# Kernel tuning notes

Hardware: AMD Instinct MI355X
Metric: run time of the kernel (lower is better)

The kernel has to match this reference:

```python
import jax, jax.numpy as jnp
import numpy as np

N, E, D, H, Z, HEADS = 20000, 160000, 3000, 512, 50, 3
EPS = 1e-5


def _bn(x, gamma, beta):
    # BatchNorm1d, training-mode stats (biased variance), eps=1e-5
    m = x.mean(axis=0)
    v = x.var(axis=0)
    return (x - m) * jax.lax.rsqrt(v + EPS) * gamma + beta


def _gat(x, src, dst, n, W, att_src, att_dst, bias, heads, c):
    # PyG GATConv, concat=False (mean over heads), negative_slope=0.2
    h = (x @ W).reshape(n, heads, c)                      # [N,H,C]
    a_s = (h * att_src).sum(-1)                           # [N,H]
    a_d = (h * att_dst).sum(-1)                           # [N,H]
    e = jax.nn.leaky_relu(a_s[src] + a_d[dst], 0.2)       # [Etot,H]
    e = e - jax.ops.segment_max(e, dst, num_segments=n)[dst]
    ex = jnp.exp(e)
    den = jax.ops.segment_sum(ex, dst, num_segments=n)[dst]
    alpha = ex / den                                      # segment softmax over incoming edges
    msg = h[src] * alpha[:, :, None]                      # [Etot,H,C]
    out = jax.ops.segment_sum(msg, dst, num_segments=n)   # [N,H,C]
    return out.mean(axis=1) + bias


def setup_inputs() -> dict:
    key = jax.random.key(0)
    ks = jax.random.split(key, 16)
    s = 0.05
    inp = {
        "x": jax.random.normal(ks[0], (N, D), dtype=jnp.float32),
        "edge_index": jax.random.randint(ks[1], (2, E), 0, N, dtype=jnp.int64),
        "W1": jax.random.normal(ks[2], (D, HEADS * H), dtype=jnp.float32) * s,
        "att_src1": jax.random.normal(ks[3], (HEADS, H), dtype=jnp.float32) * s,
        "att_dst1": jax.random.normal(ks[4], (HEADS, H), dtype=jnp.float32) * s,
        "b1": jnp.zeros((H,), jnp.float32),
        "bn1_g": jnp.ones((H,), jnp.float32),
        "bn1_b": jnp.zeros((H,), jnp.float32),
        "W2": jax.random.normal(ks[5], (H, HEADS * Z), dtype=jnp.float32) * s,
        "att_src2": jax.random.normal(ks[6], (HEADS, Z), dtype=jnp.float32) * s,
        "att_dst2": jax.random.normal(ks[7], (HEADS, Z), dtype=jnp.float32) * s,
        "b2": jnp.zeros((Z,), jnp.float32),
        "bn2_g": jnp.ones((Z,), jnp.float32),
        "bn2_b": jnp.zeros((Z,), jnp.float32),
        "lin1_w": jax.random.normal(ks[8], (H, Z), dtype=jnp.float32) * s,
        "lin1_b": jnp.zeros((H,), jnp.float32),
        "dbn_g": jnp.ones((H,), jnp.float32),
        "dbn_b": jnp.zeros((H,), jnp.float32),
        "lin2_w": jax.random.normal(ks[9], (D, H), dtype=jnp.float32) * s,
        "lin2_b": jnp.zeros((D,), jnp.float32),
    }
    return inp


def reference(x, edge_index, W1, att_src1, att_dst1, b1, bn1_g, bn1_b,
              W2, att_src2, att_dst2, b2, bn2_g, bn2_b,
              lin1_w, lin1_b, dbn_g, dbn_b, lin2_w, lin2_b):
    n = x.shape[0]
    loop = jnp.arange(n, dtype=edge_index.dtype)
    src = jnp.concatenate([edge_index[0], loop])  # add self-loops (PyG default)
    dst = jnp.concatenate([edge_index[1], loop])
    h = jax.nn.relu(_bn(_gat(x, src, dst, n, W1, att_src1, att_dst1, b1, HEADS, H), bn1_g, bn1_b))
    z = jax.nn.relu(_bn(_gat(h, src, dst, n, W2, att_src2, att_dst2, b2, HEADS, Z), bn2_g, bn2_b))
    d = jax.nn.relu(_bn(z @ lin1_w.T + lin1_b, dbn_g, dbn_b))
    out = jax.nn.relu(d @ lin2_w.T + lin2_b)
    return out
```

## Files before the change

kernel.cpp:

```cpp
#include <hip/hip_runtime.h>
#include <stdint.h>

typedef unsigned short u16;
typedef __attribute__((ext_vector_type(8))) short s16x8;
typedef __attribute__((ext_vector_type(4))) short s16x4;
typedef __attribute__((ext_vector_type(4))) float f32x4;

#define DEVFN static __device__ __forceinline__

static constexpr int NN = 20000;
static constexpr int EE = 160000;
static constexpr int ET = 180000;
static constexpr int DD = 3000;
static constexpr int HH = 512;
static constexpr int ZZ = 50;
static constexpr int C1 = 1536;
static constexpr int C2 = 150;
static constexpr int KP1 = 3008;

DEVFN u16 f2b(float f) {
  uint32_t u = __builtin_bit_cast(uint32_t, f);
  u += 0x7FFFu + ((u >> 16) & 1u);
  return (u16)(u >> 16);
}
DEVFN float b2f(u16 b) {
  uint32_t u = ((uint32_t)b) << 16;
  return __builtin_bit_cast(float, u);
}
DEVFN int edge_at(const void* ei, int mode32, long idx) {
  return mode32 ? ((const int*)ei)[idx] : (int)((const long long*)ei)[idx];
}

typedef __attribute__((address_space(1))) const unsigned int gas_uint;
typedef __attribute__((address_space(3))) unsigned int las_uint;
DEVFN void async16(const u16* g, u16* l) {
  __builtin_amdgcn_global_load_lds((gas_uint*)(uintptr_t)g,
                                   (las_uint*)(unsigned)(uintptr_t)l, 16, 0, 0);
}

__global__ void k_detect(const int* __restrict__ ei, int* __restrict__ mode) {
  __shared__ int nz;
  if (threadIdx.x == 0) nz = 0;
  __syncthreads();
  int loc = 0;
  for (int i = threadIdx.x; i < 1024; i += blockDim.x)
    if (ei[2 * i + 1] != 0) loc = 1;
  if (loc) atomicOr(&nz, 1);
  __syncthreads();
  if (threadIdx.x == 0) *mode = nz;
}

__global__ void k_deg(const void* ei, const int* __restrict__ mode, int* __restrict__ deg) {
  int m = *mode;
  long i = (long)blockIdx.x * blockDim.x + threadIdx.x;
  long st = (long)gridDim.x * blockDim.x;
  for (; i < ET; i += st) {
    int d = (i < EE) ? edge_at(ei, m, EE + i) : (int)(i - EE);
    if ((unsigned)d < (unsigned)NN) atomicAdd(&deg[d], 1);
  }
}

__global__ void k_scan_blk(const int* __restrict__ deg, int* __restrict__ rowptr,
                           int* __restrict__ bsum) {
  __shared__ int buf[256];
  int b = blockIdx.x, tid = threadIdx.x;
  int i = b * 256 + tid;
  buf[tid] = (i < NN) ? deg[i] : 0;
  __syncthreads();
  for (int off = 1; off < 256; off <<= 1) {
    int t = (tid >= off) ? buf[tid - off] : 0;
    __syncthreads();
    buf[tid] += t;
    __syncthreads();
  }
  if (i < NN) rowptr[i + 1] = buf[tid];
  if (tid == 255) bsum[b] = buf[255];
}
__global__ void k_scan_top(int* __restrict__ bsum, int nb) {
  __shared__ int buf[128];
  int tid = threadIdx.x;
  buf[tid] = (tid < nb) ? bsum[tid] : 0;
  __syncthreads();
  for (int off = 1; off < 128; off <<= 1) {
    int t = (tid >= off) ? buf[tid - off] : 0;
    __syncthreads();
    buf[tid] += t;
    __syncthreads();
  }
  if (tid < nb) bsum[tid] = buf[tid];
}
__global__ void k_scan_add(int* __restrict__ rowptr, const int* __restrict__ bsum) {
  int b = blockIdx.x, tid = threadIdx.x;
  int i = b * 256 + tid;
  if (i == 0) rowptr[0] = 0;
  if (b > 0 && i < NN) rowptr[i + 1] += bsum[b - 1];
}

__global__ void k_fill(const void* ei, const int* __restrict__ mode,
                       const int* __restrict__ rowptr, int* __restrict__ cursor,
                       int* __restrict__ srcp) {
  int m = *mode;
  long i = (long)blockIdx.x * blockDim.x + threadIdx.x;
  long st = (long)gridDim.x * blockDim.x;
  for (; i < ET; i += st) {
    int s, d;
    if (i < EE) { s = edge_at(ei, m, i); d = edge_at(ei, m, EE + i); }
    else { s = d = (int)(i - EE); }
    if ((unsigned)d < (unsigned)NN && (unsigned)s < (unsigned)NN) {
      int pos = atomicAdd(&cursor[d], 1);
      srcp[rowptr[d] + pos] = s;
    }
  }
}

__global__ void k_cvt_pad4(const float* __restrict__ in, u16* __restrict__ out,
                           int R, int Cin, int ldo) {
  int r = blockIdx.y;
  int c = (blockIdx.x * blockDim.x + threadIdx.x) * 4;
  if (c >= ldo) return;
  s16x4 o;
  const float* src = in + (size_t)r * Cin + c;
  if (r < R && c + 4 <= Cin && ((((size_t)r * Cin + c) & 3) == 0)) {
    f32x4 v = *(const f32x4*)src;
#pragma unroll
    for (int j = 0; j < 4; j++) o[j] = (short)f2b(v[j]);
  } else {
#pragma unroll
    for (int j = 0; j < 4; j++)
      o[j] = (short)((r < R && c + j < Cin) ? f2b(src[j]) : (u16)0);
  }
  *(s16x4*)(out + (size_t)r * ldo + c) = o;
}

__global__ void k_transpose_tile(const float* __restrict__ in, u16* __restrict__ out,
                                 int R, int Cc, int ldo) {
  __shared__ float t[32][33];
  int tx = threadIdx.x & 31, ty = threadIdx.x >> 5;
  int c0 = blockIdx.x * 32, r0 = blockIdx.y * 32;
#pragma unroll
  for (int j = 0; j < 4; j++) {
    int r = r0 + ty + j * 8, c = c0 + tx;
    t[ty + j * 8][tx] = (r < R && c < Cc) ? in[(size_t)r * Cc + c] : 0.f;
  }
  __syncthreads();
#pragma unroll
  for (int j = 0; j < 4; j++) {
    int c = c0 + ty + j * 8, r = r0 + tx;
    if (c < Cc && r < ldo) out[(size_t)c * ldo + r] = f2b(t[tx][ty + j * 8]);
  }
}

__global__ void k_transpose_cvt2(const float* __restrict__ in, u16* __restrict__ out,
                                 int R, int C, int Cp, int ldo) {
  long total = (long)Cp * ldo;
  long i = (long)blockIdx.x * blockDim.x + threadIdx.x;
  long st = (long)gridDim.x * blockDim.x;
  for (; i < total; i += st) {
    int c = (int)(i / ldo), r = (int)(i % ldo);
    out[i] = (c < C && r < R) ? f2b(in[(size_t)r * C + c]) : (u16)0;
  }
}

template<bool OUT_BF16, bool RELU>
__global__ __launch_bounds__(256) void k_gemm3(
    const u16* __restrict__ Ag, const u16* __restrict__ Bg, void* __restrict__ Cg,
    const float* __restrict__ bias, int M, int Nn, int Kp, int ld, int ldc) {
  __shared__ __align__(16) u16 As[2][128][64];
  __shared__ __align__(16) u16 Bs[2][128][64];
  int tid = threadIdx.x;
  int lane = tid & 63, wid = tid >> 6;
  int wm = wid >> 1, wn = wid & 1;
  int lr = lane & 15, lg = lane >> 4;

  int nwg = gridDim.x * gridDim.y;
  int wg = blockIdx.y * gridDim.x + blockIdx.x;
  int q = nwg >> 3, r = nwg & 7;
  int xcd = wg & 7, loc = wg >> 3;
  int swz = (xcd < r ? xcd * (q + 1) : r * (q + 1) + (xcd - r) * q) + loc;
  int m0 = (swz / gridDim.x) * 128, n0 = (swz % gridDim.x) * 128;

  int srow = lane >> 3;
  int skk = ((lane & 7) ^ srow) * 8;
  const u16* agp[4];
  const u16* bgp[4];
#pragma unroll
  for (int i = 0; i < 4; i++) {
    int ra = wid * 32 + i * 8 + srow;
    int ga = m0 + ra; if (ga > M - 1) ga = M - 1;
    agp[i] = Ag + (size_t)ga * ld + skk;
    bgp[i] = Bg + (size_t)(n0 + ra) * ld + skk;
  }

#define STAGE(bufi, kofs) do {                                   \
    u16* la_ = &As[bufi][0][0] + wid * 2048;                     \
    u16* lb_ = &Bs[bufi][0][0] + wid * 2048;                     \
    _Pragma("unroll")                                            \
    for (int i_ = 0; i_ < 4; i_++) {                             \
      async16(agp[i_] + (kofs), la_ + i_ * 512);                 \
      async16(bgp[i_] + (kofs), lb_ + i_ * 512);                 \
    }                                                            \
  } while (0)

  f32x4 acc[4][4];
#pragma unroll
  for (int mi = 0; mi < 4; mi++)
#pragma unroll
    for (int ni = 0; ni < 4; ni++) {
      acc[mi][ni][0] = 0.f; acc[mi][ni][1] = 0.f; acc[mi][ni][2] = 0.f; acc[mi][ni][3] = 0.f;
    }

  int rx = lr & 7;
  int NT = Kp >> 6;
  STAGE(0, 0);
  for (int t = 0; t < NT; t++) {
    int cur = t & 1;
    if (t + 1 < NT) {
      STAGE(cur ^ 1, (t + 1) * 64);
      asm volatile("s_waitcnt vmcnt(8)" ::: "memory");
    } else {
      asm volatile("s_waitcnt vmcnt(0)" ::: "memory");
    }
    __builtin_amdgcn_s_barrier();
    asm volatile("" ::: "memory");
#pragma unroll
    for (int ks = 0; ks < 2; ks++) {
      int ch = ((ks * 4 + lg) ^ rx) * 8;
      s16x8 a[4], b[4];
#pragma unroll
      for (int mi = 0; mi < 4; mi++)
        a[mi] = *(const s16x8*)&As[cur][wm * 64 + mi * 16 + lr][ch];
#pragma unroll
      for (int ni = 0; ni < 4; ni++)
        b[ni] = *(const s16x8*)&Bs[cur][wn * 64 + ni * 16 + lr][ch];
#pragma unroll
      for (int mi = 0; mi < 4; mi++)
#pragma unroll
        for (int ni = 0; ni < 4; ni++)
          acc[mi][ni] = __builtin_amdgcn_mfma_f32_16x16x32_bf16(a[mi], b[ni], acc[mi][ni], 0, 0, 0);
    }
    asm volatile("" ::: "memory");
    __builtin_amdgcn_s_barrier();
  }
#undef STAGE

#pragma unroll
  for (int mi = 0; mi < 4; mi++)
#pragma unroll
    for (int ni = 0; ni < 4; ni++) {
      int col = n0 + wn * 64 + ni * 16 + lr;
      if (col >= Nn) continue;
      float bv = bias ? bias[col] : 0.f;
#pragma unroll
      for (int j = 0; j < 4; j++) {
        int row = m0 + wm * 64 + mi * 16 + lg * 4 + j;
        if (row >= M) continue;
        float v = acc[mi][ni][j] + bv;
        if (RELU) v = v > 0.f ? v : 0.f;
        if (OUT_BF16) ((u16*)Cg)[(size_t)row * ldc + col] = f2b(v);
        else          ((float*)Cg)[(size_t)row * ldc + col] = v;
      }
    }
}

__global__ void k_attdot1b(const u16* __restrict__ h1b, const float* __restrict__ asrc,
                           const float* __restrict__ adst, float* __restrict__ as_,
                           float* __restrict__ ad_, float* __restrict__ z0,
                           float* __restrict__ z1) {
  int n = blockIdx.x;
  if (n == 0) {
    for (int i = threadIdx.x; i < HH; i += 192) { z0[i] = 0.f; z1[i] = 0.f; }
  }
  int hd = threadIdx.x >> 6, lane = threadIdx.x & 63;
  s16x8 h = *(const s16x8*)(h1b + (size_t)n * C1 + hd * 512 + lane * 8);
  const float* ap = asrc + hd * 512 + lane * 8;
  const float* dp = adst + hd * 512 + lane * 8;
  f32x4 a0 = *(const f32x4*)ap, a1 = *(const f32x4*)(ap + 4);
  f32x4 d0 = *(const f32x4*)dp, d1 = *(const f32x4*)(dp + 4);
  float ps = 0.f, pd = 0.f;
#pragma unroll
  for (int j = 0; j < 4; j++) {
    float hv = b2f((u16)h[j]);
    ps += hv * a0[j]; pd += hv * d0[j];
    float hw = b2f((u16)h[j + 4]);
    ps += hw * a1[j]; pd += hw * d1[j];
  }
  for (int off = 32; off; off >>= 1) { ps += __shfl_xor(ps, off); pd += __shfl_xor(pd, off); }
  if (lane == 0) { as_[3 * n + hd] = ps; ad_[3 * n + hd] = pd; }
}

__global__ void k_attdot2(const float* __restrict__ s2, const float* __restrict__ asrc,
                          const float* __restrict__ adst, float* __restrict__ as_,
                          float* __restrict__ ad_, float* __restrict__ z0,
                          float* __restrict__ z1, float* __restrict__ z2,
                          float* __restrict__ z3) {
  int n = blockIdx.x, tid = threadIdx.x;
  if (n == 0) {
    for (int i = tid; i < HH; i += 64) { z2[i] = 0.f; z3[i] = 0.f; }
    if (tid < 50) { z0[tid] = 0.f; z1[tid] = 0.f; }
  }
  for (int hd = 0; hd < 3; hd++) {
    float ps = 0.f, pd = 0.f;
    if (tid < 50) {
      float v = s2[(size_t)n * C2 + hd * 50 + tid];
      ps = v * asrc[hd * 50 + tid];
      pd = v * adst[hd * 50 + tid];
    }
    for (int off = 32; off; off >>= 1) { ps += __shfl_xor(ps, off); pd += __shfl_xor(pd, off); }
    if (tid == 0) { as_[3 * n + hd] = ps; ad_[3 * n + hd] = pd; }
  }
}

__global__ __launch_bounds__(192) void k_gat1(
    const u16* __restrict__ h1b, const float* __restrict__ as1,
    const float* __restrict__ ad1, const int* __restrict__ rowptr,
    const int* __restrict__ srcp, const float* __restrict__ bias,
    float* __restrict__ out) {
  int n = blockIdx.x, tid = threadIdx.x;
  __shared__ float sm[3], sden[3];
  __shared__ int s_src[128];
  __shared__ float s_alpha[128][3];
  __shared__ float part[3][512];
  int r0 = rowptr[n], deg = rowptr[n + 1] - r0;
  float adl[3] = {ad1[3 * n], ad1[3 * n + 1], ad1[3 * n + 2]};

  if (tid < 64) {
    float mx[3] = {-1e30f, -1e30f, -1e30f};
    for (int e = tid; e < deg; e += 64) {
      int s = srcp[r0 + e];
#pragma unroll
      for (int hd = 0; hd < 3; hd++) {
        float v = as1[3 * s + hd] + adl[hd];
        v = v > 0.f ? v : 0.2f * v;
        mx[hd] = fmaxf(mx[hd], v);
      }
    }
#pragma unroll
    for (int hd = 0; hd < 3; hd++)
      for (int off = 32; off; off >>= 1) mx[hd] = fmaxf(mx[hd], __shfl_xor(mx[hd], off));
    float sd[3] = {0.f, 0.f, 0.f};
    for (int e = tid; e < deg; e += 64) {
      int s = srcp[r0 + e];
#pragma unroll
      for (int hd = 0; hd < 3; hd++) {
        float v = as1[3 * s + hd] + adl[hd];
        v = v > 0.f ? v : 0.2f * v;
        sd[hd] += __expf(v - mx[hd]);
      }
    }
#pragma unroll
    for (int hd = 0; hd < 3; hd++)
      for (int off = 32; off; off >>= 1) sd[hd] += __shfl_xor(sd[hd], off);
    if (tid == 0) {
#pragma unroll
      for (int hd = 0; hd < 3; hd++) { sm[hd] = mx[hd]; sden[hd] = sd[hd]; }
    }
  }
  __syncthreads();

  int hd = tid >> 6, lane = tid & 63;
  float a[8];
#pragma unroll
  for (int j = 0; j < 8; j++) a[j] = 0.f;

  for (int base = 0; base < deg; base += 128) {
    int cnt = min(128, deg - base);
    if (tid < cnt) {
      int s = srcp[r0 + base + tid];
      s_src[tid] = s;
#pragma unroll
      for (int h2 = 0; h2 < 3; h2++) {
        float v = as1[3 * s + h2] + adl[h2];
        v = v > 0.f ? v : 0.2f * v;
        s_alpha[tid][h2] = __expf(v - sm[h2]) / sden[h2];
      }
    }
    __syncthreads();
    int e = 0;
    for (; e + 2 <= cnt; e += 2) {
      const u16* p0 = h1b + (size_t)s_src[e] * C1 + (hd << 9) + lane * 8;
      const u16* p1 = h1b + (size_t)s_src[e + 1] * C1 + (hd << 9) + lane * 8;
      s16x8 v0 = *(const s16x8*)p0;
      s16x8 v1 = *(const s16x8*)p1;
      float al0 = s_alpha[e][hd], al1 = s_alpha[e + 1][hd];
#pragma unroll
      for (int j = 0; j < 8; j++)
        a[j] += al0 * b2f((u16)v0[j]) + al1 * b2f((u16)v1[j]);
    }
    if (e < cnt) {
      const u16* p0 = h1b + (size_t)s_src[e] * C1 + (hd << 9) + lane * 8;
      s16x8 v0 = *(const s16x8*)p0;
      float al0 = s_alpha[e][hd];
#pragma unroll
      for (int j = 0; j < 8; j++) a[j] += al0 * b2f((u16)v0[j]);
    }
    __syncthreads();
  }

#pragma unroll
  for (int j = 0; j < 8; j++) part[hd][lane * 8 + j] = a[j];
  __syncthreads();
  if (tid < 128) {
    f32x4 p0 = *(const f32x4*)&part[0][tid * 4];
    f32x4 p1 = *(const f32x4*)&part[1][tid * 4];
    f32x4 p2 = *(const f32x4*)&part[2][tid * 4];
    f32x4 bv = *(const f32x4*)(bias + tid * 4);
    f32x4 o;
#pragma unroll
    for (int j = 0; j < 4; j++) o[j] = (p0[j] + p1[j] + p2[j]) * (1.f / 3.f) + bv[j];
    *(f32x4*)(out + (size_t)n * 512 + tid * 4) = o;
  }
}

__global__ void k_gat2(const float* __restrict__ s2, const float* __restrict__ as2,
                       const float* __restrict__ ad2, const int* __restrict__ rowptr,
                       const int* __restrict__ srcp, const float* __restrict__ bias,
                       float* __restrict__ z) {
  int n = blockIdx.x, tid = threadIdx.x;
  __shared__ int s_src[64];
  __shared__ float s_alpha[64][3];
  int r0 = rowptr[n], deg = rowptr[n + 1] - r0;
  float adl[3] = {ad2[3 * n], ad2[3 * n + 1], ad2[3 * n + 2]};

  float mx[3] = {-1e30f, -1e30f, -1e30f};
  for (int e = tid; e < deg; e += 64) {
    int s = srcp[r0 + e];
#pragma unroll
    for (int hd = 0; hd < 3; hd++) {
      float v = as2[3 * s + hd] + adl[hd];
      v = v > 0.f ? v : 0.2f * v;
      mx[hd] = fmaxf(mx[hd], v);
    }
  }
#pragma unroll
  for (int hd = 0; hd < 3; hd++)
    for (int off = 32; off; off >>= 1) mx[hd] = fmaxf(mx[hd], __shfl_xor(mx[hd], off));
  float sd[3] = {0.f, 0.f, 0.f};
  for (int e = tid; e < deg; e += 64) {
    int s = srcp[r0 + e];
#pragma unroll
    for (int hd = 0; hd < 3; hd++) {
      float v = as2[3 * s + hd] + adl[hd];
      v = v > 0.f ? v : 0.2f * v;
      sd[hd] += __expf(v - mx[hd]);
    }
  }
#pragma unroll
  for (int hd = 0; hd < 3; hd++)
    for (int off = 32; off; off >>= 1) sd[hd] += __shfl_xor(sd[hd], off);

  float acc = 0.f;
  for (int base = 0; base < deg; base += 64) {
    int cnt = min(64, deg - base);
    if (tid < cnt) {
      int s = srcp[r0 + base + tid];
      s_src[tid] = s;
#pragma unroll
      for (int hd = 0; hd < 3; hd++) {
        float v = as2[3 * s + hd] + adl[hd];
        v = v > 0.f ? v : 0.2f * v;
        s_alpha[tid][hd] = __expf(v - mx[hd]) / sd[hd];
      }
    }
    __syncthreads();
    if (tid < 50) {
      for (int e = 0; e < cnt; e++) {
        const float* row = s2 + (size_t)s_src[e] * C2;
#pragma unroll
        for (int hd = 0; hd < 3; hd++) acc += s_alpha[e][hd] * row[hd * 50 + tid];
      }
    }
    __syncthreads();
  }
  if (tid < 50) z[(size_t)n * ZZ + tid] = acc * (1.f / 3.f) + bias[tid];
}

__global__ void k_colstats3(const float* __restrict__ x, float* __restrict__ gsum,
                            float* __restrict__ gsq, long total, int C) {
  long i = (long)blockIdx.x * blockDim.x + threadIdx.x;
  long st = (long)gridDim.x * blockDim.x;
  int c = (int)(i % C);
  float s = 0.f, q = 0.f;
  for (; i < total; i += st) { float v = x[i]; s += v; q += v * v; }
  atomicAdd(&gsum[c], s);
  atomicAdd(&gsq[c], q);
}

__global__ void k_bnfinal(const float* __restrict__ gsum, const float* __restrict__ gsq,
                          const float* __restrict__ g, const float* __restrict__ b,
                          float* __restrict__ scale, float* __restrict__ shift,
                          int C, float invN) {
  int c = blockIdx.x * blockDim.x + threadIdx.x;
  if (c < C) {
    float m = gsum[c] * invN;
    float var = gsq[c] * invN - m * m;
    float rs = rsqrtf(var + 1e-5f);
    float sc = g[c] * rs;
    scale[c] = sc;
    shift[c] = b[c] - m * sc;
  }
}

__global__ void k_bnrelu4(const float* __restrict__ x, const float* __restrict__ sc,
                          const float* __restrict__ sh, u16* __restrict__ out, long total4) {
  long i = (long)blockIdx.x * blockDim.x + threadIdx.x;
  long st = (long)gridDim.x * blockDim.x;
  for (; i < total4; i += st) {
    long b = i * 4;
    int c = (int)(b & 511);
    f32x4 v = *(const f32x4*)(x + b);
    f32x4 s = *(const f32x4*)(sc + c);
    f32x4 t = *(const f32x4*)(sh + c);
    s16x4 o;
#pragma unroll
    for (int j = 0; j < 4; j++) {
      float r = v[j] * s[j] + t[j];
      r = r > 0.f ? r : 0.f;
      o[j] = (short)f2b(r);
    }
    *(s16x4*)(out + b) = o;
  }
}

__global__ void k_bnrelu_pad(const float* __restrict__ x, const float* __restrict__ sc,
                             const float* __restrict__ sh, u16* __restrict__ out) {
  int i = blockIdx.x * blockDim.x + threadIdx.x;
  if (i >= NN * 64) return;
  int c = i & 63, r = i >> 6;
  float v = 0.f;
  if (c < 50) {
    v = x[r * 50 + c] * sc[c] + sh[c];
    v = v > 0.f ? v : 0.f;
  }
  out[i] = f2b(v);
}

extern "C" void kernel_launch(void* const* d_in, const int* in_sizes, int n_in,
                              void* d_out, int out_size, void* d_ws, size_t ws_size,
                              hipStream_t stream) {
  (void)in_sizes; (void)n_in; (void)out_size;
  const float* x     = (const float*)d_in[0];
  const void*  ei    = d_in[1];
  const float* W1    = (const float*)d_in[2];
  const float* asrc1 = (const float*)d_in[3];
  const float* adst1 = (const float*)d_in[4];
  const float* b1    = (const float*)d_in[5];
  const float* bn1g  = (const float*)d_in[6];
  const float* bn1b  = (const float*)d_in[7];
  const float* W2    = (const float*)d_in[8];
  const float* asrc2 = (const float*)d_in[9];
  const float* adst2 = (const float*)d_in[10];
  const float* b2    = (const float*)d_in[11];
  const float* bn2g  = (const float*)d_in[12];
  const float* bn2b  = (const float*)d_in[13];
  const float* l1w   = (const float*)d_in[14];
  const float* l1b   = (const float*)d_in[15];
  const float* dbng  = (const float*)d_in[16];
  const float* dbnb  = (const float*)d_in[17];
  const float* l2w   = (const float*)d_in[18];
  const float* l2b   = (const float*)d_in[19];
  float* out = (float*)d_out;
  char* ws = (char*)d_ws;

  size_t off = 0;
  auto alloc = [&](size_t b) { size_t r = off; off += (b + 255) & ~(size_t)255; return r; };
  const size_t oXB  = alloc(120320000);
  const size_t oH1  = alloc(61440000);
  const size_t oW1T = alloc((size_t)C1 * KP1 * 2);
  const size_t oAS1 = alloc((size_t)NN * 12), oAD1 = alloc((size_t)NN * 12);
  const size_t oAS2 = alloc((size_t)NN * 12), oAD2 = alloc((size_t)NN * 12);
  const size_t oRP  = alloc((size_t)(NN + 1) * 4);
  const size_t oDEG = alloc((size_t)NN * 4);
  const size_t oSRC = alloc((size_t)ET * 4);
  const size_t oMODE = alloc(256);
  const size_t oBSUM = alloc(512);
  const size_t oS1 = alloc(2048), oQ1 = alloc(2048);
  const size_t oS2 = alloc(2048), oQ2 = alloc(2048);
  const size_t oS3 = alloc(2048), oQ3 = alloc(2048);
  const size_t oSC = alloc(2048), oSH = alloc(2048);
  if (ws_size < off) return;

  u16*   xb   = (u16*)(ws + oXB);
  float* g1   = (float*)(ws + oXB);
  u16*   h2b  = (u16*)(ws + oXB + 40960000);
  float* s2   = (float*)(ws + oXB + 61440000);
  float* zf   = (float*)(ws + oXB + 73440000);
  u16*   zb   = (u16*)(ws + oXB + 77440000);
  u16*   w2T  = (u16*)(ws + oXB + 80000000);
  u16*   l1wT = (u16*)(ws + oXB + 80262400);
  u16*   l2wT = (u16*)(ws + oXB + 80328192);
  float* dbuf = (float*)(ws + oXB);
  u16*   h1b  = (u16*)(ws + oH1);
  u16*   db   = (u16*)(ws + oH1);
  u16*   w1T  = (u16*)(ws + oW1T);
  int* mode   = (int*)(ws + oMODE);
  int* bsum   = (int*)(ws + oBSUM);
  int* deg    = (int*)(ws + oDEG);
  int* rowptr = (int*)(ws + oRP);
  int* srcp   = (int*)(ws + oSRC);
  float *as1 = (float*)(ws + oAS1), *ad1 = (float*)(ws + oAD1);
  float *as2 = (float*)(ws + oAS2), *ad2 = (float*)(ws + oAD2);
  float *sum1 = (float*)(ws + oS1), *sq1 = (float*)(ws + oQ1);
  float *sum2 = (float*)(ws + oS2), *sq2 = (float*)(ws + oQ2);
  float *sum3 = (float*)(ws + oS3), *sq3 = (float*)(ws + oQ3);
  float *bsc = (float*)(ws + oSC), *bsh = (float*)(ws + oSH);

  k_detect<<<1, 256, 0, stream>>>((const int*)ei, mode);
  hipMemsetAsync(deg, 0, (size_t)NN * 4, stream);
  k_deg<<<512, 256, 0, stream>>>(ei, mode, deg);
  k_scan_blk<<<79, 256, 0, stream>>>(deg, rowptr, bsum);
  k_scan_top<<<1, 128, 0, stream>>>(bsum, 79);
  k_scan_add<<<79, 256, 0, stream>>>(rowptr, bsum);
  hipMemsetAsync(deg, 0, (size_t)NN * 4, stream);
  k_fill<<<512, 256, 0, stream>>>(ei, mode, rowptr, deg, srcp);

  k_cvt_pad4<<<dim3(3, NN), 256, 0, stream>>>(x, xb, NN, DD, KP1);
  k_transpose_tile<<<dim3(C1 / 32, KP1 / 32), 256, 0, stream>>>(W1, w1T, DD, C1, KP1);
  k_gemm3<true, false><<<dim3(12, 157), 256, 0, stream>>>(xb, w1T, h1b, nullptr,
                                                          NN, C1, KP1, KP1, C1);
  k_attdot1b<<<NN, 192, 0, stream>>>(h1b, asrc1, adst1, as1, ad1, sum1, sq1);
  k_gat1<<<NN, 192, 0, stream>>>(h1b, as1, ad1, rowptr, srcp, b1, g1);
  k_colstats3<<<512, 256, 0, stream>>>(g1, sum1, sq1, (long)NN * HH, HH);
  k_bnfinal<<<2, 256, 0, stream>>>(sum1, sq1, bn1g, bn1b, bsc, bsh, HH, 1.0f / NN);
  k_bnrelu4<<<2048, 256, 0, stream>>>(g1, bsc, bsh, h2b, (long)NN * HH / 4);

  k_transpose_cvt2<<<256, 256, 0, stream>>>(W2, w2T, HH, C2, 256, HH);
  k_gemm3<false, false><<<dim3(2, 157), 256, 0, stream>>>(h2b, w2T, s2, nullptr,
                                                          NN, C2, HH, HH, C2);
  k_attdot2<<<NN, 64, 0, stream>>>(s2, asrc2, adst2, as2, ad2, sum2, sq2, sum3, sq3);
  k_gat2<<<NN, 64, 0, stream>>>(s2, as2, ad2, rowptr, srcp, b2, zf);
  k_colstats3<<<25, 256, 0, stream>>>(zf, sum2, sq2, (long)NN * ZZ, ZZ);
  k_bnfinal<<<1, 64, 0, stream>>>(sum2, sq2, bn2g, bn2b, bsc, bsh, ZZ, 1.0f / NN);
  k_bnrelu_pad<<<5000, 256, 0, stream>>>(zf, bsc, bsh, zb);

  k_cvt_pad4<<<dim3(1, HH), 256, 0, stream>>>(l1w, l1wT, HH, ZZ, 64);
  k_gemm3<false, false><<<dim3(4, 157), 256, 0, stream>>>(zb, l1wT, dbuf, l1b,
                                                          NN, HH, 64, 64, HH);
  k_colstats3<<<512, 256, 0, stream>>>(dbuf, sum3, sq3, (long)NN * HH, HH);
  k_bnfinal<<<2, 256, 0, stream>>>(sum3, sq3, dbng, dbnb, bsc, bsh, HH, 1.0f / NN);
  k_bnrelu4<<<2048, 256, 0, stream>>>(dbuf, bsc, bsh, db, (long)NN * HH / 4);
  k_cvt_pad4<<<dim3(1, 3072), 256, 0, stream>>>(l2w, l2wT, DD, HH, HH);
  k_gemm3<false, true><<<dim3(24, 157), 256, 0, stream>>>(db, l2wT, out, l2b,
                                                          NN, DD, HH, HH, DD);
}
```

Measured before the change: 807.7 us.

## Add 256x256-tile 8-wave phased MFMA GEMM for the two large GEMMs

Adds a new bf16 MFMA GEMM kernel with 256x256 output tiles and 512 threads (8 waves). It double-buffers A/B tiles in LDS with XOR swizzling and splits each K-step into four phases that interleave async global-to-LDS loads, barriers and prioritized MFMA bursts. The first GATConv projection and the final decoder linear layer now use it in place of the 128x128 kernel, aiming for more data reuse per tile and better overlap of loads with compute. To make the K-tile count even, the padded K of W1 grows to 3072 while x keeps a 3008 stride, so the last K tile reads past each x row. That relies on zero-padded weights, and the final x row's read runs slightly beyond the buffer.

After: 724.3 us. 10.3% less time.

```diff
diff --git a/kernel.cpp b/kernel.cpp
--- a/kernel.cpp
+++ b/kernel.cpp
@@ -16,7 +16,8 @@
 static constexpr int ZZ = 50;
 static constexpr int C1 = 1536;
 static constexpr int C2 = 150;
-static constexpr int KP1 = 3008;
+static constexpr int KA1 = 3008;
+static constexpr int KP1 = 3072;
 
 DEVFN u16 f2b(float f) {
   uint32_t u = __builtin_bit_cast(uint32_t, f);
@@ -159,6 +160,143 @@
     int c = (int)(i / ldo), r = (int)(i % ldo);
     out[i] = (c < C && r < R) ? f2b(in[(size_t)r * C + c]) : (u16)0;
   }
+}
+
+template<bool OUT_BF16, bool RELU>
+__global__ __launch_bounds__(512, 2) void k_gemm8(
+    const u16* __restrict__ Ag, const u16* __restrict__ Bg, void* __restrict__ Cg,
+    const float* __restrict__ bias, int M, int Nn, int Kp, int lda, int ldb, int ldc) {
+  __shared__ __align__(16) u16 As[2][256][64];
+  __shared__ __align__(16) u16 Bs[2][256][64];
+  int tid = threadIdx.x;
+  int lane = tid & 63, wid = tid >> 6;
+  int wm = wid >> 2, wn = wid & 3;
+  int lr = lane & 15, lg = lane >> 4;
+  int rx = lr & 7;
+
+  int nwg = gridDim.x * gridDim.y;
+  int wg = blockIdx.y * gridDim.x + blockIdx.x;
+  int q = nwg >> 3, r = nwg & 7;
+  int xcd = wg & 7, loc = wg >> 3;
+  int swz = (xcd < r ? xcd * (q + 1) : r * (q + 1) + (xcd - r) * q) + loc;
+  int m0 = (swz / gridDim.x) * 256, n0 = (swz % gridDim.x) * 256;
+
+  int srow = tid >> 3;
+  int schunk = ((tid & 7) ^ (srow & 7)) * 8;
+  const u16* agp[4];
+  const u16* bgp[4];
+#pragma unroll
+  for (int i = 0; i < 4; i++) {
+    int ra = i * 64 + srow;
+    int ga = m0 + ra; if (ga > M - 1) ga = M - 1;
+    agp[i] = Ag + (size_t)ga * lda + schunk;
+    bgp[i] = Bg + (size_t)(n0 + ra) * ldb + schunk;
+  }
+  u16* aB0 = &As[0][0][0]; u16* aB1 = &As[1][0][0];
+  u16* bB0 = &Bs[0][0][0]; u16* bB1 = &Bs[1][0][0];
+
+#define SA(cb, h, kt) do {                                                  \
+    u16* d_ = ((cb) ? aB1 : aB0);                                           \
+    async16(agp[2*(h)]   + (size_t)(kt)*64, d_ + (2*(h))*4096 + wid*512);   \
+    async16(agp[2*(h)+1] + (size_t)(kt)*64, d_ + (2*(h)+1)*4096 + wid*512); \
+  } while (0)
+#define SB(cb, h, kt) do {                                                  \
+    u16* d_ = ((cb) ? bB1 : bB0);                                           \
+    async16(bgp[2*(h)]   + (size_t)(kt)*64, d_ + (2*(h))*4096 + wid*512);   \
+    async16(bgp[2*(h)+1] + (size_t)(kt)*64, d_ + (2*(h)+1)*4096 + wid*512); \
+  } while (0)
+#define BARX() do { asm volatile("" ::: "memory");                          \
+    __builtin_amdgcn_s_barrier(); asm volatile("" ::: "memory"); } while (0)
+#define VMC4() asm volatile("s_waitcnt vmcnt(4)" ::: "memory")
+#define RDA(dst, cb, mi, ks) dst = *(const s16x8*)&As[cb][wm*128+(mi)*16+lr][(((ks)*4+lg)^rx)*8]
+#define RDB(dst, cb, ni, ks) dst = *(const s16x8*)&Bs[cb][wn*64+(ni)*16+lr][(((ks)*4+lg)^rx)*8]
+
+  f32x4 acc[8][4];
+#pragma unroll
+  for (int mi = 0; mi < 8; mi++)
+#pragma unroll
+    for (int ni = 0; ni < 4; ni++) {
+      acc[mi][ni][0] = 0.f; acc[mi][ni][1] = 0.f;
+      acc[mi][ni][2] = 0.f; acc[mi][ni][3] = 0.f;
+    }
+
+  s16x8 bfr[2][4];
+  s16x8 fA0, fA1, fB0, fB1;
+
+#define DO_MFMA(P) do {                                                         \
+    _Pragma("unroll")                                                           \
+    for (int ni_ = 0; ni_ < 4; ni_++) {                                         \
+      acc[2*(P)][ni_]   = __builtin_amdgcn_mfma_f32_16x16x32_bf16(fA0, bfr[0][ni_], acc[2*(P)][ni_], 0, 0, 0);   \
+      acc[2*(P)][ni_]   = __builtin_amdgcn_mfma_f32_16x16x32_bf16(fA1, bfr[1][ni_], acc[2*(P)][ni_], 0, 0, 0);   \
+      acc[2*(P)+1][ni_] = __builtin_amdgcn_mfma_f32_16x16x32_bf16(fB0, bfr[0][ni_], acc[2*(P)+1][ni_], 0, 0, 0); \
+      acc[2*(P)+1][ni_] = __builtin_amdgcn_mfma_f32_16x16x32_bf16(fB1, bfr[1][ni_], acc[2*(P)+1][ni_], 0, 0, 0); \
+    } } while (0)
+
+#define PHASE(cb, P, STAGE_STMT, VM_STMT) do {                                  \
+    if ((P) == 0) {                                                             \
+      RDB(bfr[0][0], cb, 0, 0); RDB(bfr[0][1], cb, 1, 0);                       \
+      RDB(bfr[0][2], cb, 2, 0); RDB(bfr[0][3], cb, 3, 0);                       \
+      RDB(bfr[1][0], cb, 0, 1); RDB(bfr[1][1], cb, 1, 1);                       \
+      RDB(bfr[1][2], cb, 2, 1); RDB(bfr[1][3], cb, 3, 1);                       \
+    }                                                                           \
+    RDA(fA0, cb, 2*(P), 0);   RDA(fA1, cb, 2*(P), 1);                           \
+    RDA(fB0, cb, 2*(P)+1, 0); RDA(fB1, cb, 2*(P)+1, 1);                         \
+    STAGE_STMT;                                                                 \
+    BARX();                                                                     \
+    __builtin_amdgcn_s_setprio(1);                                              \
+    DO_MFMA(P);                                                                 \
+    __builtin_amdgcn_s_setprio(0);                                              \
+    VM_STMT;                                                                    \
+    BARX();                                                                     \
+  } while (0)
+
+  int nt = Kp >> 6;
+  SB(0, 0, 0); SB(0, 1, 0);
+  SA(0, 0, 0); SA(0, 1, 0);
+  { int k1 = 1 < nt ? 1 : nt - 1; SB(1, 0, k1); SB(1, 1, k1); }
+  VMC4();
+  BARX();
+
+  for (int t = 0; t < nt; t += 2) {
+    int t2 = (t + 2 < nt) ? t + 2 : nt - 1;
+    int t3 = (t + 3 < nt) ? t + 3 : nt - 1;
+    PHASE(0, 0, SA(1, 0, t + 1), (void)0);
+    PHASE(0, 1, SA(1, 1, t + 1), (void)0);
+    PHASE(0, 2, SB(0, 0, t2),    (void)0);
+    PHASE(0, 3, SB(0, 1, t2),    VMC4());
+    PHASE(1, 0, SA(0, 0, t2),    (void)0);
+    PHASE(1, 1, SA(0, 1, t2),    (void)0);
+    PHASE(1, 2, SB(1, 0, t3),    (void)0);
+    PHASE(1, 3, SB(1, 1, t3),    VMC4());
+  }
+  asm volatile("s_waitcnt vmcnt(0)" ::: "memory");
+
+#undef SA
+#undef SB
+#undef BARX
+#undef VMC4
+#undef RDA
+#undef RDB
+#undef DO_MFMA
+#undef PHASE
+
+#pragma unroll
+  for (int mi = 0; mi < 8; mi++)
+#pragma unroll
+    for (int ni = 0; ni < 4; ni++) {
+      int col = n0 + wn * 64 + ni * 16 + lr;
+      if (col >= Nn) continue;
+      float bv = bias ? bias[col] : 0.f;
+#pragma unroll
+      for (int j = 0; j < 4; j++) {
+        int row = m0 + wm * 128 + mi * 16 + lg * 4 + j;
+        if (row >= M) continue;
+        float v = acc[mi][ni][j] + bv;
+        if (RELU) v = v > 0.f ? v : 0.f;
+        if (OUT_BF16) ((u16*)Cg)[(size_t)row * ldc + col] = f2b(v);
+        else          ((float*)Cg)[(size_t)row * ldc + col] = v;
+      }
+    }
 }
 
 template<bool OUT_BF16, bool RELU>
@@ -613,10 +751,10 @@
   hipMemsetAsync(deg, 0, (size_t)NN * 4, stream);
   k_fill<<<512, 256, 0, stream>>>(ei, mode, rowptr, deg, srcp);
 
-  k_cvt_pad4<<<dim3(3, NN), 256, 0, stream>>>(x, xb, NN, DD, KP1);
+  k_cvt_pad4<<<dim3(3, NN), 256, 0, stream>>>(x, xb, NN, DD, KA1);
   k_transpose_tile<<<dim3(C1 / 32, KP1 / 32), 256, 0, stream>>>(W1, w1T, DD, C1, KP1);
-  k_gemm3<true, false><<<dim3(12, 157), 256, 0, stream>>>(xb, w1T, h1b, nullptr,
-                                                          NN, C1, KP1, KP1, C1);
+  k_gemm8<true, false><<<dim3(6, 79), 512, 0, stream>>>(xb, w1T, h1b, nullptr,
+                                                        NN, C1, KP1, KA1, KP1, C1);
   k_attdot1b<<<NN, 192, 0, stream>>>(h1b, asrc1, adst1, as1, ad1, sum1, sq1);
   k_gat1<<<NN, 192, 0, stream>>>(h1b, as1, ad1, rowptr, srcp, b1, g1);
   k_colstats3<<<512, 256, 0, stream>>>(g1, sum1, sq1, (long)NN * HH, HH);
@@ -639,6 +777,6 @@
   k_bnfinal<<<2, 256, 0, stream>>>(sum3, sq3, dbng, dbnb, bsc, bsh, HH, 1.0f / NN);
   k_bnrelu4<<<2048, 256, 0, stream>>>(dbuf, bsc, bsh, db, (long)NN * HH / 4);
   k_cvt_pad4<<<dim3(1, 3072), 256, 0, stream>>>(l2w, l2wT, DD, HH, HH);
-  k_gemm3<false, true><<<dim3(24, 157), 256, 0, stream>>>(db, l2wT, out, l2b,
-                                                          NN, DD, HH, HH, DD);
-}
+  k_gemm8<false, true><<<dim3(12, 79), 512, 0, stream>>>(db, l2wT, out, l2b,
+                                                         NN, DD, 512, HH, HH, DD);
+}
```
